# Performance work log

Hardware: AMD Instinct MI355X
Metric: run time of the kernel (lower is better)

## Reference

```python
import jax, jax.numpy as jnp
import numpy as np

B, S, HIST, D, NH, L = 8, 1024, 128, 1024, 16, 6
SD, TD, AD = 10, 3, 5
DH = D // NH
FF = 4 * D
EPS = 1e-5
SCALE = 1.0 / np.sqrt(DH)


def posenc(T):
    # sinusoidal PE, matches PositionalEncoding (positions start at 0)
    pos = jnp.arange(T, dtype=jnp.float32)[:, None]
    div = jnp.exp(jnp.arange(0, D, 2, dtype=jnp.float32) * (-np.log(10000.0) / D))
    pe = jnp.zeros((T, D), jnp.float32)
    pe = pe.at[:, 0::2].set(jnp.sin(pos * div))
    pe = pe.at[:, 1::2].set(jnp.cos(pos * div))
    return pe


def layernorm(x, g, b):
    m = jnp.mean(x, -1, keepdims=True)
    v = jnp.var(x, -1, keepdims=True)
    return (x - m) * jax.lax.rsqrt(v + EPS) * g + b


def mlp2(u, w1, b1, w2, b2):
    # Linear -> SiLU -> Linear (ConditionEmbedding branch)
    return jax.nn.silu(u @ w1 + b1) @ w2 + b2


def mha(q_in, kv_in, wq, bq, wk, bk, wv, bv, wo, bo, mask):
    Bq, Tq, _ = q_in.shape
    Tk = kv_in.shape[1]
    q = (q_in @ wq + bq).reshape(Bq, Tq, NH, DH)
    k = (kv_in @ wk + bk).reshape(Bq, Tk, NH, DH)
    v = (kv_in @ wv + bv).reshape(Bq, Tk, NH, DH)
    s = jnp.einsum('bthd,bshd->bhts', q, k) * SCALE + mask
    a = jax.nn.softmax(s, axis=-1)
    o = jnp.einsum('bhts,bshd->bthd', a, v).reshape(Bq, Tq, D)
    return o @ wo + bo


def setup_inputs():
    key = jax.random.key(0)
    ki = iter(jax.random.split(key, 64))
    w = lambda *sh: jax.random.normal(next(ki), sh, jnp.float32) * 0.02
    z = lambda *sh: jnp.zeros(sh, jnp.float32)
    inp = {
        'x': jax.random.normal(next(ki), (B, S, SD), jnp.float32),
        't': jax.random.randint(next(ki), (B,), 0, 30, dtype=jnp.int32),
        'target': jax.random.normal(next(ki), (B, TD), jnp.float32),
        'action': jax.random.normal(next(ki), (B, AD), jnp.float32),
        'history': jax.random.normal(next(ki), (B, HIST, SD), jnp.float32),
        'in_w': w(SD, D), 'in_b': z(D),
        't_w1': w(1, D), 't_b1': z(D), 't_w2': w(D, D), 't_b2': z(D),
        'tg_w1': w(TD, D), 'tg_b1': z(D), 'tg_w2': w(D, D), 'tg_b2': z(D),
        'ac_w1': w(AD, D), 'ac_b1': z(D), 'ac_w2': w(D, D), 'ac_b2': z(D),
        'sa_wq': w(L, D, D), 'sa_bq': z(L, D), 'sa_wk': w(L, D, D), 'sa_bk': z(L, D),
        'sa_wv': w(L, D, D), 'sa_bv': z(L, D), 'sa_wo': w(L, D, D), 'sa_bo': z(L, D),
        'ca_wq': w(L, D, D), 'ca_bq': z(L, D), 'ca_wk': w(L, D, D), 'ca_bk': z(L, D),
        'ca_wv': w(L, D, D), 'ca_bv': z(L, D), 'ca_wo': w(L, D, D), 'ca_bo': z(L, D),
        'ln1_g': jnp.ones((L, D), jnp.float32), 'ln1_b': z(L, D),
        'ln2_g': jnp.ones((L, D), jnp.float32), 'ln2_b': z(L, D),
        'ln3_g': jnp.ones((L, D), jnp.float32), 'ln3_b': z(L, D),
        'ff_w1': w(L, D, FF), 'ff_b1': z(L, FF), 'ff_w2': w(L, FF, D), 'ff_b2': z(L, D),
        'out_w': w(D, SD), 'out_b': z(SD),
    }
    return inp


def reference(x, t, target, action, history, in_w, in_b,
              t_w1, t_b1, t_w2, t_b2, tg_w1, tg_b1, tg_w2, tg_b2,
              ac_w1, ac_b1, ac_w2, ac_b2,
              sa_wq, sa_bq, sa_wk, sa_bk, sa_wv, sa_bv, sa_wo, sa_bo,
              ca_wq, ca_bq, ca_wk, ca_bk, ca_wv, ca_bv, ca_wo, ca_bo,
              ln1_g, ln1_b, ln2_g, ln2_b, ln3_g, ln3_b,
              ff_w1, ff_b1, ff_w2, ff_b2, out_w, out_b):
    # embed current traj and history (PE applied to each separately, as in torch code)
    x_emb = x @ in_w + in_b + posenc(S)[None]
    h_emb = history @ in_w + in_b + posenc(HIST)[None]
    # condition embedding: t + target + action branches
    cond = (mlp2(t[:, None].astype(jnp.float32), t_w1, t_b1, t_w2, t_b2)
            + mlp2(target, tg_w1, tg_b1, tg_w2, tg_b2)
            + mlp2(action, ac_w1, ac_b1, ac_w2, ac_b2))
    z = jnp.concatenate([h_emb, x_emb], axis=1) + cond[:, None, :]  # [B, T, D]
    T = HIST + S
    mask = jnp.where(jnp.tril(jnp.ones((T, T), bool)), 0.0, -jnp.inf)[None, None]
    mem = z  # TransformerDecoder memory is the (fixed) input sequence
    for i in range(L):
        # post-LN TransformerDecoderLayer: self-attn, cross-attn, relu FFN
        z = layernorm(z + mha(z, z, sa_wq[i], sa_bq[i], sa_wk[i], sa_bk[i],
                              sa_wv[i], sa_bv[i], sa_wo[i], sa_bo[i], mask), ln1_g[i], ln1_b[i])
        z = layernorm(z + mha(z, mem, ca_wq[i], ca_bq[i], ca_wk[i], ca_bk[i],
                              ca_wv[i], ca_bv[i], ca_wo[i], ca_bo[i], mask), ln2_g[i], ln2_b[i])
        ff = jax.nn.relu(z @ ff_w1[i] + ff_b1[i]) @ ff_w2[i] + ff_b2[i]
        z = layernorm(z + ff, ln3_g[i], ln3_b[i])
    return z[:, -S:, :] @ out_w + out_b
```

## Files before the change

### kernel.cpp

```cpp
#include <hip/hip_runtime.h>
#include <hip/hip_bf16.h>
#include <stdint.h>

#define B_    8
#define S_    1024
#define HIST_ 128
#define T_    1152
#define D_    1024
#define NH_   16
#define DH_   64
#define FF_   4096
#define L_    6
#define NROWS_ (B_*T_)

typedef __attribute__((ext_vector_type(8))) __bf16 bf16x8;
typedef __attribute__((ext_vector_type(4))) __bf16 bf16x4;
typedef __attribute__((ext_vector_type(4))) float  f32x4;

static __device__ __forceinline__ f32x4 mfma16(bf16x8 a, bf16x8 b, f32x4 c) {
  return __builtin_amdgcn_mfma_f32_16x16x32_bf16(a, b, c, 0, 0, 0);
}
static __device__ __forceinline__ void gload16(const __bf16* g, __bf16* l) {
  __builtin_amdgcn_global_load_lds((const __attribute__((address_space(1))) void*)g,
                                   (__attribute__((address_space(3))) void*)l, 16, 0, 0);
}
static __device__ __forceinline__ int xcd_swz(int orig, int nwg) {
  const int q = nwg >> 3, r = nwg & 7;
  const int x = orig & 7, i = orig >> 3;
  return (x < r ? x*(q+1) : r*(q+1) + (x-r)*q) + i;
}

template<int OUTMODE, int RELU>
__global__ __launch_bounds__(256) void gemm_k(const __bf16* __restrict__ A,
                                              const __bf16* __restrict__ Bt,
                                              const float* __restrict__ b1,
                                              const float* __restrict__ b2,
                                              const float* __restrict__ b3, int s1, int s2,
                                              void* __restrict__ CoutRM,
                                              __bf16* __restrict__ CoutT,
                                              int M, int N, int K, int ldc, int tsplit) {
  __shared__ __align__(16) __bf16 As[128*32];
  __shared__ __align__(16) __bf16 Bs[128*32];
  const int tid = threadIdx.x;
  const int wv = tid >> 6, ln = tid & 63;
  const int nbx = N >> 7;
  const int wg = xcd_swz(blockIdx.x, gridDim.x);
  const int m0 = (wg / nbx) * 128, n0 = (wg % nbx) * 128;
  const int wr = wv >> 1, wc = wv & 1;
  const int srow = wv*32 + (ln>>2);
  const int scol = (ln&3)*8;
  const __bf16* ga0 = A  + (size_t)(m0 + srow)*K + scol;
  const __bf16* gb0 = Bt + (size_t)(n0 + srow)*K + scol;
  __bf16* la0 = As + (wv*32)*32;
  __bf16* lb0 = Bs + (wv*32)*32;
  const f32x4 zero = {0.f,0.f,0.f,0.f};
  f32x4 acc[4][4];
#pragma unroll
  for (int i=0;i<4;i++)
#pragma unroll
    for (int j=0;j<4;j++) acc[i][j] = zero;
  for (int kt = 0; kt < K; kt += 32) {
    gload16(ga0 + kt,                  la0);
    gload16(ga0 + kt + (size_t)16*K,   la0 + 512);
    gload16(gb0 + kt,                  lb0);
    gload16(gb0 + kt + (size_t)16*K,   lb0 + 512);
    __syncthreads();
    const __bf16* ap = As + (wr*64 + (ln&15))*32 + (ln>>4)*8;
    const __bf16* bp = Bs + (wc*64 + (ln&15))*32 + (ln>>4)*8;
    bf16x8 af[4], bfr[4];
#pragma unroll
    for (int i=0;i<4;i++) { af[i] = *(const bf16x8*)(ap + i*512); bfr[i] = *(const bf16x8*)(bp + i*512); }
#pragma unroll
    for (int mi=0;mi<4;mi++)
#pragma unroll
      for (int ni=0;ni<4;ni++)
        acc[mi][ni] = mfma16(af[mi], bfr[ni], acc[mi][ni]);
    __syncthreads();
  }
  const int colb = n0 + wc*64 + (ln&15);
#pragma unroll
  for (int mi=0;mi<4;mi++) {
    const int row = m0 + wr*64 + mi*16 + ((ln>>4)<<2);
#pragma unroll
    for (int ni=0;ni<4;ni++) {
      const int col = colb + ni*16;
      const float bv = (col < s1) ? b1[col] : ((col < s2) ? b2[col-s1] : b3[col-s2]);
      if (OUTMODE == 2 || (OUTMODE == 3 && col >= tsplit)) {
        bf16x4 ct;
#pragma unroll
        for (int j=0;j<4;j++) {
          float v = acc[mi][ni][j] + bv;
          if (RELU) v = fmaxf(v, 0.f);
          ct[j] = (__bf16)v;
        }
        const int tc = (OUTMODE == 3) ? col - tsplit : col;
        *(bf16x4*)(CoutT + (size_t)tc*M + row) = ct;
      } else {
#pragma unroll
        for (int j=0;j<4;j++) {
          float v = acc[mi][ni][j] + bv;
          if (RELU) v = fmaxf(v, 0.f);
          if (OUTMODE == 0) ((float*)CoutRM)[(size_t)(row+j)*ldc + col] = v;
          else              ((__bf16*)CoutRM)[(size_t)(row+j)*ldc + col] = (__bf16)v;
        }
      }
    }
  }
}

__global__ __launch_bounds__(256) void attn_k(const __bf16* __restrict__ QK,
                                              const __bf16* __restrict__ Vt,
                                              __bf16* __restrict__ O) {
  __shared__ __align__(16) __bf16 Ks[2][4096];
  __shared__ __align__(16) __bf16 Vs[2][4096];
  __shared__ __align__(16) __bf16 Pl[4][32*72];
  const int tid = threadIdx.x;
  const int wv = tid >> 6, ln = tid & 63;
  const int l15 = ln & 15, g = ln >> 4;
  const int wg = xcd_swz(blockIdx.x, 1152);
  const int qb = 8 - (wg % 9);
  const int hd = (wg / 9) & 15;
  const int b  = wg / 144;
  const int q0 = qb*128 + wv*32;

  bf16x8 qf[2][2];
#pragma unroll
  for (int f=0; f<2; ++f)
#pragma unroll
    for (int h=0; h<2; ++h)
      qf[f][h] = *(const bf16x8*)(QK + (size_t)(b*T_ + q0 + f*16 + l15)*2048 + hd*64 + h*32 + g*8);

  const int sr = tid >> 3;
  const int si = tid & 7;
  const int cb0 = (si*16) ^ ((sr & 7) << 4);
  const char* kg = (const char*)(QK + (size_t)b*T_*2048 + 1024 + hd*64);
  const char* vg = (const char*)(Vt + (size_t)hd*64*NROWS_ + (size_t)b*T_);

  const f32x4 zero = {0.f,0.f,0.f,0.f};
  f32x4 o[2][4];
#pragma unroll
  for (int f=0; f<2; ++f)
#pragma unroll
    for (int d=0; d<4; ++d) o[f][d] = zero;
  float mrun[2] = {-3.0e38f, -3.0e38f};
  float lrun[2] = {0.f, 0.f};
  const int nt = 2*qb + 2;

  {
    const int c = 0, kt = 0;
#pragma unroll
    for (int hr=0; hr<2; ++hr) {
      const int r = sr + hr*32;
      gload16((const __bf16*)(kg + (size_t)(kt + r)*4096 + cb0), &Ks[c][0] + hr*2048 + wv*512);
      gload16((const __bf16*)(vg + (size_t)r*(NROWS_*2) + (size_t)kt*2 + cb0), &Vs[c][0] + hr*2048 + wv*512);
    }
  }

  for (int t = 0; t < nt; ++t) {
    __syncthreads();
    if (t+1 < nt) {
      const int c = (t+1)&1, kt2 = (t+1)*64;
#pragma unroll
      for (int hr=0; hr<2; ++hr) {
        const int r = sr + hr*32;
        gload16((const __bf16*)(kg + (size_t)(kt2 + r)*4096 + cb0), &Ks[c][0] + hr*2048 + wv*512);
        gload16((const __bf16*)(vg + (size_t)r*(NROWS_*2) + (size_t)kt2*2 + cb0), &Vs[c][0] + hr*2048 + wv*512);
      }
    }
    const int kt = t*64;
    if (kt > q0 + 31) continue;
    const char* ks = (const char*)&Ks[t&1][0];
    const char* vs = (const char*)&Vs[t&1][0];

#pragma unroll
    for (int f=0; f<2; ++f) {
      const int qrow = q0 + f*16 + l15;
      f32x4 st[4];
      __builtin_amdgcn_s_setprio(1);
#pragma unroll
      for (int kf=0; kf<4; ++kf) {
        const int row = kf*16 + l15;
        const int sw = (row & 7) << 4;
        const bf16x8 k0 = *(const bf16x8*)(ks + row*128 + ((g*16) ^ sw));
        const bf16x8 k1 = *(const bf16x8*)(ks + row*128 + ((64 + g*16) ^ sw));
        st[kf] = mfma16(k1, qf[f][1], mfma16(k0, qf[f][0], zero));
      }
      __builtin_amdgcn_s_setprio(0);
      float p[16];
#pragma unroll
      for (int kf=0; kf<4; ++kf)
#pragma unroll
        for (int r=0; r<4; ++r) {
          const int kgl = kt + kf*16 + g*4 + r;
          p[kf*4+r] = (kgl <= qrow) ? st[kf][r]*0.125f : -3.0e38f;
        }
      float mloc = p[0];
#pragma unroll
      for (int i=1;i<16;i++) mloc = fmaxf(mloc, p[i]);
      mloc = fmaxf(mloc, __shfl_xor(mloc, 16));
      mloc = fmaxf(mloc, __shfl_xor(mloc, 32));
      const float mnew = fmaxf(mrun[f], mloc);
      const float corr = __expf(mrun[f] - mnew);
      float ls = 0.f;
#pragma unroll
      for (int i=0;i<16;i++) { p[i] = __expf(p[i] - mnew); ls += p[i]; }
      ls += __shfl_xor(ls, 16); ls += __shfl_xor(ls, 32);
      lrun[f] = lrun[f]*corr + ls;
      mrun[f] = mnew;
#pragma unroll
      for (int kf=0; kf<4; ++kf) {
        bf16x4 pw;
#pragma unroll
        for (int r=0;r<4;r++) pw[r] = (__bf16)p[kf*4+r];
        *(bf16x4*)(&Pl[wv][(f*16 + l15)*72 + kf*16 + g*4]) = pw;
      }
      float cr[4];
#pragma unroll
      for (int r=0;r<4;r++) cr[r] = __shfl(corr, g*4 + r);
#pragma unroll
      for (int db=0; db<4; ++db)
#pragma unroll
        for (int r=0;r<4;r++) o[f][db][r] *= cr[r];
    }
    __builtin_amdgcn_s_setprio(1);
#pragma unroll
    for (int f=0; f<2; ++f)
#pragma unroll
      for (int ks2=0; ks2<2; ++ks2) {
        const bf16x8 pa = *(const bf16x8*)(&Pl[wv][(f*16 + l15)*72 + ks2*32 + g*8]);
#pragma unroll
        for (int db=0; db<4; ++db) {
          const int d = db*16 + l15;
          const bf16x8 vf = *(const bf16x8*)(vs + d*128 + ((ks2*64 + g*16) ^ ((d & 7) << 4)));
          o[f][db] = mfma16(pa, vf, o[f][db]);
        }
      }
    __builtin_amdgcn_s_setprio(0);
  }

#pragma unroll
  for (int f=0; f<2; ++f) {
    const float inv = 1.f / lrun[f];
    float ir[4];
#pragma unroll
    for (int r=0;r<4;r++) ir[r] = __shfl(inv, g*4 + r);
#pragma unroll
    for (int db=0; db<4; ++db)
#pragma unroll
      for (int r=0;r<4;r++)
        O[(size_t)(b*T_ + q0 + f*16 + g*4 + r)*D_ + hd*64 + db*16 + l15] = (__bf16)(o[f][db][r]*ir[r]);
  }
}

__global__ __launch_bounds__(256) void wprep_k(const float* __restrict__ q, const float* __restrict__ k,
                                               const float* __restrict__ v, const float* __restrict__ o,
                                               const float* __restrict__ cq, const float* __restrict__ ck,
                                               const float* __restrict__ cv, const float* __restrict__ co,
                                               const float* __restrict__ f1, const float* __restrict__ f2,
                                               __bf16* __restrict__ wb) {
  __shared__ float tile[32][33];
  const int id = blockIdx.x;
  const float* src; __bf16* dst; int R, C, bx, by;
  if (id < 8192) {
    const int m = id >> 10, t = id & 1023; bx = t & 31; by = t >> 5;
    const float* srcs[8] = {q,k,v,o,cq,ck,cv,co};
    src = srcs[m]; dst = wb + (size_t)m*1048576; R = 1024; C = 1024;
  } else if (id < 12288) {
    const int t = id - 8192; bx = t & 127; by = t >> 7;
    src = f1; dst = wb + (size_t)8*1048576; R = 1024; C = 4096;
  } else {
    const int t = id - 12288; bx = t & 31; by = t >> 5;
    src = f2; dst = wb + (size_t)12*1048576; R = 4096; C = 1024;
  }
  const int tx = threadIdx.x & 31, ty = threadIdx.x >> 5;
  const int r0 = by*32, c0 = bx*32;
#pragma unroll
  for (int i=0;i<4;i++) tile[ty+i*8][tx] = src[(size_t)(r0+ty+i*8)*C + c0+tx];
  __syncthreads();
#pragma unroll
  for (int i=0;i<4;i++) dst[(size_t)(c0+ty+i*8)*R + r0+tx] = (__bf16)tile[tx][ty+i*8];
}

__global__ __launch_bounds__(256) void ln_k(const float* __restrict__ zin, const float* __restrict__ yin,
                                            const float* __restrict__ gam, const float* __restrict__ bet,
                                            float* __restrict__ zout, __bf16* __restrict__ zbout) {
  const int row = blockIdx.x, tid = threadIdx.x;
  const f32x4 zv = ((const f32x4*)(zin + (size_t)row*D_))[tid];
  const f32x4 yv = ((const f32x4*)(yin + (size_t)row*D_))[tid];
  f32x4 v = zv + yv;
  float s1 = v[0]+v[1]+v[2]+v[3];
  float s2 = v[0]*v[0]+v[1]*v[1]+v[2]*v[2]+v[3]*v[3];
#pragma unroll
  for (int off=32; off; off>>=1) { s1 += __shfl_xor(s1,off); s2 += __shfl_xor(s2,off); }
  __shared__ float red[8];
  const int wv = tid>>6, ln = tid&63;
  if (ln==0) { red[wv] = s1; red[4+wv] = s2; }
  __syncthreads();
  s1 = red[0]+red[1]+red[2]+red[3];
  s2 = red[4]+red[5]+red[6]+red[7];
  const float mean = s1 * (1.f/1024.f);
  const float var = s2 * (1.f/1024.f) - mean*mean;
  const float rs = rsqrtf(var + 1e-5f);
  const f32x4 gv = ((const f32x4*)gam)[tid];
  const f32x4 bv = ((const f32x4*)bet)[tid];
  f32x4 r; bf16x4 rb;
#pragma unroll
  for (int j=0;j<4;j++) { float t = (v[j]-mean)*rs*gv[j] + bv[j]; r[j] = t; rb[j] = (__bf16)t; }
  ((f32x4*)(zout + (size_t)row*D_))[tid] = r;
  ((bf16x4*)(zbout + (size_t)row*D_))[tid] = rb;
}

__global__ __launch_bounds__(256) void cond1_k(const int* __restrict__ t, const float* __restrict__ target,
                                               const float* __restrict__ action,
                                               const float* __restrict__ t_w1, const float* __restrict__ t_b1,
                                               const float* __restrict__ tg_w1, const float* __restrict__ tg_b1,
                                               const float* __restrict__ ac_w1, const float* __restrict__ ac_b1,
                                               float* __restrict__ h3) {
  const int i = blockIdx.x*256 + threadIdx.x;
  const int b = i >> 10, d = i & 1023;
  float u = (float)t[b] * t_w1[d] + t_b1[d];
  h3[i] = u / (1.f + __expf(-u));
  u = tg_b1[d];
#pragma unroll
  for (int j=0;j<3;j++) u += target[b*3+j]*tg_w1[j*1024+d];
  h3[8192 + i] = u / (1.f + __expf(-u));
  u = ac_b1[d];
#pragma unroll
  for (int j=0;j<5;j++) u += action[b*5+j]*ac_w1[j*1024+d];
  h3[16384 + i] = u / (1.f + __expf(-u));
}

__global__ __launch_bounds__(256) void cond2_k(const float* __restrict__ h3,
                                               const float* __restrict__ t_w2, const float* __restrict__ tg_w2,
                                               const float* __restrict__ ac_w2, float* __restrict__ cpart) {
  const int i = blockIdx.x*256 + threadIdx.x;
  const int ks = blockIdx.y;
  const int b = i >> 10, d = i & 1023;
  const float* ht = h3 + b*1024;
  const float* hg = h3 + 8192 + b*1024;
  const float* ha = h3 + 16384 + b*1024;
  float a = 0.f;
  for (int k = ks*128; k < ks*128+128; ++k)
    a += ht[k]*t_w2[(size_t)k*1024+d] + hg[k]*tg_w2[(size_t)k*1024+d] + ha[k]*ac_w2[(size_t)k*1024+d];
  cpart[ks*8192 + i] = a;
}

__global__ __launch_bounds__(256) void embed_k(const float* __restrict__ x, const float* __restrict__ hist,
                                               const float* __restrict__ in_w, const float* __restrict__ in_b,
                                               const float* __restrict__ cpart,
                                               const float* __restrict__ t_b2, const float* __restrict__ tg_b2,
                                               const float* __restrict__ ac_b2,
                                               float* __restrict__ z, __bf16* __restrict__ zb,
                                               __bf16* __restrict__ memb) {
  const int row = blockIdx.x, tid = threadIdx.x;
  const int b = row / T_, tt = row - b*T_;
  const float* feat = (tt < HIST_) ? (hist + ((size_t)b*HIST_ + tt)*10) : (x + ((size_t)b*S_ + (tt-HIST_))*10);
  float f[10];
#pragma unroll
  for (int s=0;s<10;s++) f[s] = feat[s];
  const float te = (float)((tt < HIST_) ? tt : tt - HIST_);
  f32x4 a = ((const f32x4*)in_b)[tid];
#pragma unroll
  for (int u=0;u<2;u++) {
    const int d = tid*4 + 2*u;
    const float freq = __expf((float)d * (-9.210340371976184f/1024.f));
    float sn, cs;
    __sincosf(te*freq, &sn, &cs);
    a[2*u] += sn; a[2*u+1] += cs;
  }
  a += ((const f32x4*)t_b2)[tid];
  a += ((const f32x4*)tg_b2)[tid];
  a += ((const f32x4*)ac_b2)[tid];
  const int cb = b*256 + tid;
#pragma unroll
  for (int ks=0;ks<8;ks++) a += ((const f32x4*)cpart)[ks*2048 + cb];
#pragma unroll
  for (int s=0;s<10;s++) {
    const f32x4 wv = ((const f32x4*)(in_w + s*1024))[tid];
    a += wv * f[s];
  }
  ((f32x4*)(z + (size_t)row*D_))[tid] = a;
  bf16x4 ab;
#pragma unroll
  for (int j=0;j<4;j++) ab[j] = (__bf16)a[j];
  ((bf16x4*)(zb + (size_t)row*D_))[tid] = ab;
  ((bf16x4*)(memb + (size_t)row*D_))[tid] = ab;
}

__global__ __launch_bounds__(256) void outp_k(const float* __restrict__ z, const float* __restrict__ w,
                                              const float* __restrict__ bo, float* __restrict__ out) {
  const int wv = threadIdx.x>>6, ln = threadIdx.x&63;
  const int row = blockIdx.x*4 + wv;
  const int b = row >> 10, s = row & 1023;
  const float* zr = z + ((size_t)b*T_ + HIST_ + s)*D_;
  float acc[10];
#pragma unroll
  for (int o=0;o<10;o++) acc[o]=0.f;
  for (int k=ln; k<1024; k+=64) {
    const float zv = zr[k];
    const float* wr = w + k*10;
#pragma unroll
    for (int o=0;o<10;o++) acc[o] += zv*wr[o];
  }
#pragma unroll
  for (int o=0;o<10;o++) {
#pragma unroll
    for (int off=32; off; off>>=1) acc[o] += __shfl_xor(acc[o], off);
  }
  if (ln==0) {
#pragma unroll
    for (int o=0;o<10;o++) out[(size_t)row*10+o] = acc[o] + bo[o];
  }
}

extern "C" void kernel_launch(void* const* d_in, const int* in_sizes, int n_in,
                              void* d_out, int out_size, void* d_ws, size_t ws_size,
                              hipStream_t stream) {
  const float* x      = (const float*)d_in[0];
  const int*   t      = (const int*)  d_in[1];
  const float* target = (const float*)d_in[2];
  const float* action = (const float*)d_in[3];
  const float* hist   = (const float*)d_in[4];
  const float* in_w   = (const float*)d_in[5];
  const float* in_b   = (const float*)d_in[6];
  const float* t_w1   = (const float*)d_in[7];
  const float* t_b1   = (const float*)d_in[8];
  const float* t_w2   = (const float*)d_in[9];
  const float* t_b2   = (const float*)d_in[10];
  const float* tg_w1  = (const float*)d_in[11];
  const float* tg_b1  = (const float*)d_in[12];
  const float* tg_w2  = (const float*)d_in[13];
  const float* tg_b2  = (const float*)d_in[14];
  const float* ac_w1  = (const float*)d_in[15];
  const float* ac_b1  = (const float*)d_in[16];
  const float* ac_w2  = (const float*)d_in[17];
  const float* ac_b2  = (const float*)d_in[18];
  const float* sa_wq  = (const float*)d_in[19];
  const float* sa_bq  = (const float*)d_in[20];
  const float* sa_wk  = (const float*)d_in[21];
  const float* sa_bk  = (const float*)d_in[22];
  const float* sa_wv  = (const float*)d_in[23];
  const float* sa_bv  = (const float*)d_in[24];
  const float* sa_wo  = (const float*)d_in[25];
  const float* sa_bo  = (const float*)d_in[26];
  const float* ca_wq  = (const float*)d_in[27];
  const float* ca_bq  = (const float*)d_in[28];
  const float* ca_wk  = (const float*)d_in[29];
  const float* ca_bk  = (const float*)d_in[30];
  const float* ca_wv  = (const float*)d_in[31];
  const float* ca_bv  = (const float*)d_in[32];
  const float* ca_wo  = (const float*)d_in[33];
  const float* ca_bo  = (const float*)d_in[34];
  const float* ln1_g  = (const float*)d_in[35];
  const float* ln1_b  = (const float*)d_in[36];
  const float* ln2_g  = (const float*)d_in[37];
  const float* ln2_b  = (const float*)d_in[38];
  const float* ln3_g  = (const float*)d_in[39];
  const float* ln3_b  = (const float*)d_in[40];
  const float* ff_w1  = (const float*)d_in[41];
  const float* ff_b1  = (const float*)d_in[42];
  const float* ff_w2  = (const float*)d_in[43];
  const float* ff_b2  = (const float*)d_in[44];
  const float* out_w  = (const float*)d_in[45];
  const float* out_b  = (const float*)d_in[46];

  if (ws_size < (size_t)224*1024*1024) return;

  char* p = (char*)d_ws;
  auto take = [&](size_t bytes) { char* r = p; p += (bytes + 255) & ~(size_t)255; return r; };
  __bf16* wbuf = (__bf16*)take((size_t)16*1024*1024*2);
  float*  z    = (float*) take((size_t)NROWS_*D_*4);
  __bf16* zb   = (__bf16*)take((size_t)NROWS_*D_*2);
  __bf16* memb = (__bf16*)take((size_t)NROWS_*D_*2);
  __bf16* qk   = (__bf16*)take((size_t)NROWS_*2048*2);
  __bf16* vt   = (__bf16*)take((size_t)1024*NROWS_*2);
  __bf16* ob   = (__bf16*)take((size_t)NROWS_*D_*2);
  float*  y    = (float*) take((size_t)NROWS_*D_*4);
  float*  h3   = (float*) take((size_t)3*8192*4);
  float*  cpart= (float*) take((size_t)8*8192*4);
  __bf16* ffh  = qk;

  const dim3 blk(256);
  const int BIG = 1<<30;
  cond1_k<<<32, blk, 0, stream>>>(t, target, action, t_w1, t_b1, tg_w1, tg_b1, ac_w1, ac_b1, h3);
  cond2_k<<<dim3(32,8), blk, 0, stream>>>(h3, t_w2, tg_w2, ac_w2, cpart);
  embed_k<<<NROWS_, blk, 0, stream>>>(x, hist, in_w, in_b, cpart, t_b2, tg_b2, ac_b2, z, zb, memb);

  const int M = NROWS_;
  for (int li=0; li<L_; ++li) {
    const size_t w0 = (size_t)li*D_*D_, b0 = (size_t)li*D_;
    const size_t f1 = (size_t)li*D_*FF_, fb1 = (size_t)li*FF_;
    wprep_k<<<16384, blk, 0, stream>>>(sa_wq+w0, sa_wk+w0, sa_wv+w0, sa_wo+w0,
                                       ca_wq+w0, ca_wk+w0, ca_wv+w0, ca_wo+w0,
                                       ff_w1+f1, ff_w2+f1, wbuf);
    gemm_k<3,0><<<24*72, blk, 0, stream>>>(zb, wbuf+0*1048576, sa_bq+b0, sa_bk+b0, sa_bv+b0, 1024, 2048,
                                           qk, vt, M, 3072, 1024, 2048, 2048);
    attn_k<<<1152, blk, 0, stream>>>(qk, vt, ob);
    gemm_k<0,0><<<8*72, blk, 0, stream>>>(ob, wbuf+3*1048576, sa_bo+b0, sa_bo+b0, sa_bo+b0, BIG, BIG,
                                          y, vt, M, 1024, 1024, 1024, BIG);
    ln_k<<<NROWS_, blk, 0, stream>>>(z, y, ln1_g+b0, ln1_b+b0, z, zb);
    gemm_k<1,0><<<8*72, blk, 0, stream>>>(zb, wbuf+4*1048576, ca_bq+b0, ca_bq+b0, ca_bq+b0, BIG, BIG,
                                          qk, vt, M, 1024, 1024, 2048, BIG);
    gemm_k<3,0><<<16*72, blk, 0, stream>>>(memb, wbuf+5*1048576, ca_bk+b0, ca_bv+b0, ca_bv+b0, 1024, 2048,
                                           qk + 1024, vt, M, 2048, 1024, 2048, 1024);
    attn_k<<<1152, blk, 0, stream>>>(qk, vt, ob);
    gemm_k<0,0><<<8*72, blk, 0, stream>>>(ob, wbuf+7*1048576, ca_bo+b0, ca_bo+b0, ca_bo+b0, BIG, BIG,
                                          y, vt, M, 1024, 1024, 1024, BIG);
    ln_k<<<NROWS_, blk, 0, stream>>>(z, y, ln2_g+b0, ln2_b+b0, z, zb);
    gemm_k<1,1><<<32*72, blk, 0, stream>>>(zb, wbuf+(size_t)8*1048576, ff_b1+fb1, ff_b1+fb1, ff_b1+fb1, BIG, BIG,
                                           ffh, vt, M, 4096, 1024, 4096, BIG);
    gemm_k<0,0><<<8*72, blk, 0, stream>>>(ffh, wbuf+(size_t)12*1048576, ff_b2+b0, ff_b2+b0, ff_b2+b0, BIG, BIG,
                                          y, vt, M, 1024, 4096, 1024, BIG);
    ln_k<<<NROWS_, blk, 0, stream>>>(z, y, ln3_g+b0, ln3_b+b0, z, zb);
  }
  outp_k<<<2048, blk, 0, stream>>>(z, out_w, out_b, (float*)d_out);
}
```

Before: 4.663 ms.

## Replace 128x128 GEMM with double-buffered 256x256 tile kernel using swizzled LDS

Replaces the single-buffered 128x128x32 GEMM with a 512-thread 256x256x64 tile kernel. It double-buffers LDS via global_load_lds, overlapping next-tile loads with MFMA work through split-phase prefetch and explicit vmcnt waits. It also XOR-swizzles the LDS layout to avoid bank conflicts. Larger tiles cut global traffic per FLOP and synchronisation overhead, but they raise LDS use (128KB) and register pressure, and the fewer workgroups (144 for N=1024) may underfill the 256 CUs.

```diff
diff --git a/kernel.cpp b/kernel.cpp
--- a/kernel.cpp
+++ b/kernel.cpp
@@ -24,6 +24,10 @@
   __builtin_amdgcn_global_load_lds((const __attribute__((address_space(1))) void*)g,
                                    (__attribute__((address_space(3))) void*)l, 16, 0, 0);
 }
+static __device__ __forceinline__ void gload16b(const char* g, char* l) {
+  __builtin_amdgcn_global_load_lds((const __attribute__((address_space(1))) void*)g,
+                                   (__attribute__((address_space(3))) void*)l, 16, 0, 0);
+}
 static __device__ __forceinline__ int xcd_swz(int orig, int nwg) {
   const int q = nwg >> 3, r = nwg & 7;
   const int x = orig & 7, i = orig >> 3;
@@ -31,61 +35,114 @@
 }
 
 template<int OUTMODE, int RELU>
-__global__ __launch_bounds__(256) void gemm_k(const __bf16* __restrict__ A,
-                                              const __bf16* __restrict__ Bt,
-                                              const float* __restrict__ b1,
-                                              const float* __restrict__ b2,
-                                              const float* __restrict__ b3, int s1, int s2,
-                                              void* __restrict__ CoutRM,
-                                              __bf16* __restrict__ CoutT,
-                                              int M, int N, int K, int ldc, int tsplit) {
-  __shared__ __align__(16) __bf16 As[128*32];
-  __shared__ __align__(16) __bf16 Bs[128*32];
+__global__ __launch_bounds__(512, 2) void gemm256_k(const __bf16* __restrict__ A,
+                                                    const __bf16* __restrict__ Bt,
+                                                    const float* __restrict__ b1,
+                                                    const float* __restrict__ b2,
+                                                    const float* __restrict__ b3, int s1, int s2,
+                                                    void* __restrict__ CoutRM,
+                                                    __bf16* __restrict__ CoutT,
+                                                    int M, int N, int K, int ldc, int tsplit) {
+  __shared__ __align__(16) __bf16 LA[2][2][8192];
+  __shared__ __align__(16) __bf16 LB[2][2][8192];
   const int tid = threadIdx.x;
-  const int wv = tid >> 6, ln = tid & 63;
-  const int nbx = N >> 7;
+  const int wid = tid >> 6, ln = tid & 63;
+  const int wm = wid >> 2, wn = wid & 3;
+  const int l15 = ln & 15, g = ln >> 4;
+  const int nbx = N >> 8;
   const int wg = xcd_swz(blockIdx.x, gridDim.x);
-  const int m0 = (wg / nbx) * 128, n0 = (wg % nbx) * 128;
-  const int wr = wv >> 1, wc = wv & 1;
-  const int srow = wv*32 + (ln>>2);
-  const int scol = (ln&3)*8;
-  const __bf16* ga0 = A  + (size_t)(m0 + srow)*K + scol;
-  const __bf16* gb0 = Bt + (size_t)(n0 + srow)*K + scol;
-  __bf16* la0 = As + (wv*32)*32;
-  __bf16* lb0 = Bs + (wv*32)*32;
+  const int m0 = (wg / nbx) << 8, n0 = (wg % nbx) << 8;
+  const size_t rstep = (size_t)K * 2;
+  const int scb = ((tid & 7) << 4) ^ (((tid >> 5) & 1) << 5) ^ (((tid >> 6) & 1) << 6);
+  const char* gA = (const char*)A  + (size_t)(m0 + (tid >> 3)) * rstep + scb;
+  const char* gB = (const char*)Bt + (size_t)(n0 + (tid >> 3)) * rstep + scb;
+  const char* gA64  = gA + 64*rstep;
+  const char* gA128 = gA + 128*rstep;
+  const char* gA192 = gA + 192*rstep;
+  const char* gB64  = gB + 64*rstep;
+  const char* gB128 = gB + 128*rstep;
+  const char* gB192 = gB + 192*rstep;
+
   const f32x4 zero = {0.f,0.f,0.f,0.f};
-  f32x4 acc[4][4];
-#pragma unroll
-  for (int i=0;i<4;i++)
+  f32x4 acc[8][4];
+#pragma unroll
+  for (int i=0;i<8;i++)
 #pragma unroll
     for (int j=0;j<4;j++) acc[i][j] = zero;
-  for (int kt = 0; kt < K; kt += 32) {
-    gload16(ga0 + kt,                  la0);
-    gload16(ga0 + kt + (size_t)16*K,   la0 + 512);
-    gload16(gb0 + kt,                  lb0);
-    gload16(gb0 + kt + (size_t)16*K,   lb0 + 512);
-    __syncthreads();
-    const __bf16* ap = As + (wr*64 + (ln&15))*32 + (ln>>4)*8;
-    const __bf16* bp = Bs + (wc*64 + (ln&15))*32 + (ln>>4)*8;
-    bf16x8 af[4], bfr[4];
-#pragma unroll
-    for (int i=0;i<4;i++) { af[i] = *(const bf16x8*)(ap + i*512); bfr[i] = *(const bf16x8*)(bp + i*512); }
-#pragma unroll
-    for (int mi=0;mi<4;mi++)
-#pragma unroll
-      for (int ni=0;ni<4;ni++)
-        acc[mi][ni] = mfma16(af[mi], bfr[ni], acc[mi][ni]);
-    __syncthreads();
-  }
-  const int colb = n0 + wc*64 + (ln&15);
-#pragma unroll
-  for (int mi=0;mi<4;mi++) {
-    const int row = m0 + wr*64 + mi*16 + ((ln>>4)<<2);
+
+  const int sw = (((l15 >> 2) & 1) << 5) | (((l15 >> 3) & 1) << 6);
+  const int NT = K >> 6;
+
+  {
+    char* dA0 = (char*)&LA[0][0][0]; char* dB0 = (char*)&LB[0][0][0];
+    char* dA1 = (char*)&LA[0][1][0]; char* dB1 = (char*)&LB[0][1][0];
+    gload16b(gA,    dA0 + tid*16);  gload16b(gA64,  dA0 + 8192 + tid*16);
+    gload16b(gB,    dB0 + tid*16);  gload16b(gB64,  dB0 + 8192 + tid*16);
+    gload16b(gA128, dA1 + tid*16);  gload16b(gA192, dA1 + 8192 + tid*16);
+    gload16b(gB128, dB1 + tid*16);  gload16b(gB192, dB1 + 8192 + tid*16);
+  }
+
+  for (int t = 0; t < NT; ++t) {
+    const int buf = t & 1, nbuf = buf ^ 1;
+    const size_t ktb = (size_t)(t+1) << 7;
+    if (t+1 < NT) {
+      char* dA = (char*)&LA[nbuf][0][0]; char* dB = (char*)&LB[nbuf][0][0];
+      gload16b(gA   + ktb, dA + tid*16);  gload16b(gA64 + ktb, dA + 8192 + tid*16);
+      gload16b(gB   + ktb, dB + tid*16);  gload16b(gB64 + ktb, dB + 8192 + tid*16);
+      asm volatile("s_waitcnt vmcnt(4)" ::: "memory");
+    } else {
+      asm volatile("s_waitcnt vmcnt(0)" ::: "memory");
+    }
+    __builtin_amdgcn_s_barrier();
+    const char* pa = (const char*)&LA[buf][wm][0];
+    const char* pb = (const char*)&LB[buf][wn>>1][0] + (wn & 1)*8192;
+    {
+      const int cb = (g*16) ^ sw;
+      bf16x8 af[8], bfr[4];
+#pragma unroll
+      for (int mi=0;mi<8;mi++) af[mi]  = *(const bf16x8*)(pa + (mi*16 + l15)*128 + cb);
+#pragma unroll
+      for (int ni=0;ni<4;ni++) bfr[ni] = *(const bf16x8*)(pb + (ni*16 + l15)*128 + cb);
+      __builtin_amdgcn_s_setprio(1);
+#pragma unroll
+      for (int mi=0;mi<8;mi++)
+#pragma unroll
+        for (int ni=0;ni<4;ni++)
+          acc[mi][ni] = mfma16(af[mi], bfr[ni], acc[mi][ni]);
+      __builtin_amdgcn_s_setprio(0);
+    }
+    if (t+1 < NT) {
+      char* dA = (char*)&LA[nbuf][1][0]; char* dB = (char*)&LB[nbuf][1][0];
+      gload16b(gA128 + ktb, dA + tid*16);  gload16b(gA192 + ktb, dA + 8192 + tid*16);
+      gload16b(gB128 + ktb, dB + tid*16);  gload16b(gB192 + ktb, dB + 8192 + tid*16);
+    }
+    {
+      const int cb = (64 + g*16) ^ sw;
+      bf16x8 af[8], bfr[4];
+#pragma unroll
+      for (int mi=0;mi<8;mi++) af[mi]  = *(const bf16x8*)(pa + (mi*16 + l15)*128 + cb);
+#pragma unroll
+      for (int ni=0;ni<4;ni++) bfr[ni] = *(const bf16x8*)(pb + (ni*16 + l15)*128 + cb);
+      __builtin_amdgcn_s_setprio(1);
+#pragma unroll
+      for (int mi=0;mi<8;mi++)
+#pragma unroll
+        for (int ni=0;ni<4;ni++)
+          acc[mi][ni] = mfma16(af[mi], bfr[ni], acc[mi][ni]);
+      __builtin_amdgcn_s_setprio(0);
+    }
+    __builtin_amdgcn_s_barrier();
+  }
+
+  const int colb = n0 + wn*64 + l15;
+#pragma unroll
+  for (int mi=0;mi<8;mi++) {
+    const int row = m0 + wm*128 + mi*16 + g*4;
 #pragma unroll
     for (int ni=0;ni<4;ni++) {
       const int col = colb + ni*16;
       const float bv = (col < s1) ? b1[col] : ((col < s2) ? b2[col-s1] : b3[col-s2]);
-      if (OUTMODE == 2 || (OUTMODE == 3 && col >= tsplit)) {
+      if (OUTMODE == 3 && col >= tsplit) {
         bf16x4 ct;
 #pragma unroll
         for (int j=0;j<4;j++) {
@@ -93,8 +150,7 @@
           if (RELU) v = fmaxf(v, 0.f);
           ct[j] = (__bf16)v;
         }
-        const int tc = (OUTMODE == 3) ? col - tsplit : col;
-        *(bf16x4*)(CoutT + (size_t)tc*M + row) = ct;
+        *(bf16x4*)(CoutT + (size_t)(col - tsplit)*M + row) = ct;
       } else {
 #pragma unroll
         for (int j=0;j<4;j++) {
@@ -180,9 +236,9 @@
 #pragma unroll
       for (int kf=0; kf<4; ++kf) {
         const int row = kf*16 + l15;
-        const int sw = (row & 7) << 4;
-        const bf16x8 k0 = *(const bf16x8*)(ks + row*128 + ((g*16) ^ sw));
-        const bf16x8 k1 = *(const bf16x8*)(ks + row*128 + ((64 + g*16) ^ sw));
+        const int swz = (row & 7) << 4;
+        const bf16x8 k0 = *(const bf16x8*)(ks + row*128 + ((g*16) ^ swz));
+        const bf16x8 k1 = *(const bf16x8*)(ks + row*128 + ((64 + g*16) ^ swz));
         st[kf] = mfma16(k1, qf[f][1], mfma16(k0, qf[f][0], zero));
       }
       __builtin_amdgcn_s_setprio(0);
@@ -481,6 +537,7 @@
   __bf16* ffh  = qk;
 
   const dim3 blk(256);
+  const dim3 blk5(512);
   const int BIG = 1<<30;
   cond1_k<<<32, blk, 0, stream>>>(t, target, action, t_w1, t_b1, tg_w1, tg_b1, ac_w1, ac_b1, h3);
   cond2_k<<<dim3(32,8), blk, 0, stream>>>(h3, t_w2, tg_w2, ac_w2, cpart);
@@ -493,24 +550,24 @@
     wprep_k<<<16384, blk, 0, stream>>>(sa_wq+w0, sa_wk+w0, sa_wv+w0, sa_wo+w0,
                                        ca_wq+w0, ca_wk+w0, ca_wv+w0, ca_wo+w0,
                                        ff_w1+f1, ff_w2+f1, wbuf);
-    gemm_k<3,0><<<24*72, blk, 0, stream>>>(zb, wbuf+0*1048576, sa_bq+b0, sa_bk+b0, sa_bv+b0, 1024, 2048,
-                                           qk, vt, M, 3072, 1024, 2048, 2048);
+    gemm256_k<3,0><<<36*12, blk5, 0, stream>>>(zb, wbuf+0*1048576, sa_bq+b0, sa_bk+b0, sa_bv+b0, 1024, 2048,
+                                               qk, vt, M, 3072, 1024, 2048, 2048);
     attn_k<<<1152, blk, 0, stream>>>(qk, vt, ob);
-    gemm_k<0,0><<<8*72, blk, 0, stream>>>(ob, wbuf+3*1048576, sa_bo+b0, sa_bo+b0, sa_bo+b0, BIG, BIG,
-                                          y, vt, M, 1024, 1024, 1024, BIG);
+    gemm256_k<0,0><<<36*4, blk5, 0, stream>>>(ob, wbuf+3*1048576, sa_bo+b0, sa_bo+b0, sa_bo+b0, BIG, BIG,
+                                              y, vt, M, 1024, 1024, 1024, BIG);
     ln_k<<<NROWS_, blk, 0, stream>>>(z, y, ln1_g+b0, ln1_b+b0, z, zb);
-    gemm_k<1,0><<<8*72, blk, 0, stream>>>(zb, wbuf+4*1048576, ca_bq+b0, ca_bq+b0, ca_bq+b0, BIG, BIG,
-                                          qk, vt, M, 1024, 1024, 2048, BIG);
-    gemm_k<3,0><<<16*72, blk, 0, stream>>>(memb, wbuf+5*1048576, ca_bk+b0, ca_bv+b0, ca_bv+b0, 1024, 2048,
-                                           qk + 1024, vt, M, 2048, 1024, 2048, 1024);
+    gemm256_k<1,0><<<36*4, blk5, 0, stream>>>(zb, wbuf+4*1048576, ca_bq+b0, ca_bq+b0, ca_bq+b0, BIG, BIG,
+                                              qk, vt, M, 1024, 1024, 2048, BIG);
+    gemm256_k<3,0><<<36*8, blk5, 0, stream>>>(memb, wbuf+5*1048576, ca_bk+b0, ca_bv+b0, ca_bv+b0, 1024, 2048,
+                                              qk + 1024, vt, M, 2048, 1024, 2048, 1024);
     attn_k<<<1152, blk, 0, stream>>>(qk, vt, ob);
-    gemm_k<0,0><<<8*72, blk, 0, stream>>>(ob, wbuf+7*1048576, ca_bo+b0, ca_bo+b0, ca_bo+b0, BIG, BIG,
-                                          y, vt, M, 1024, 1024, 1024, BIG);
+    gemm256_k<0,0><<<36*4, blk5, 0, stream>>>(ob, wbuf+7*1048576, ca_bo+b0, ca_bo+b0, ca_bo+b0, BIG, BIG,
+                                              y, vt, M, 1024, 1024, 1024, BIG);
     ln_k<<<NROWS_, blk, 0, stream>>>(z, y, ln2_g+b0, ln2_b+b0, z, zb);
-    gemm_k<1,1><<<32*72, blk, 0, stream>>>(zb, wbuf+(size_t)8*1048576, ff_b1+fb1, ff_b1+fb1, ff_b1+fb1, BIG, BIG,
-                                           ffh, vt, M, 4096, 1024, 4096, BIG);
-    gemm_k<0,0><<<8*72, blk, 0, stream>>>(ffh, wbuf+(size_t)12*1048576, ff_b2+b0, ff_b2+b0, ff_b2+b0, BIG, BIG,
-                                          y, vt, M, 1024, 4096, 1024, BIG);
+    gemm256_k<1,1><<<36*16, blk5, 0, stream>>>(zb, wbuf+(size_t)8*1048576, ff_b1+fb1, ff_b1+fb1, ff_b1+fb1, BIG, BIG,
+                                               ffh, vt, M, 4096, 1024, 4096, BIG);
+    gemm256_k<0,0><<<36*4, blk5, 0, stream>>>(ffh, wbuf+(size_t)12*1048576, ff_b2+b0, ff_b2+b0, ff_b2+b0, BIG, BIG,
+                                              y, vt, M, 1024, 4096, 1024, BIG);
     ln_k<<<NROWS_, blk, 0, stream>>>(z, y, ln3_g+b0, ln3_b+b0, z, zb);
   }
   outp_k<<<2048, blk, 0, stream>>>(z, out_w, out_b, (float*)d_out);
```

Result: slower. 4.850 ms (+4.0%).
